# Kernel tuning notes

Hardware: AMD Instinct MI355X
Metric: run time of the kernel (lower is better)

The kernel has to match this reference:

```python
import jax, jax.numpy as jnp
import numpy as np

EPS_NORM = 1e-12  # F.normalize eps
BN_EPS = 1e-5     # BatchNorm2d eps
N_NODES = 18
T_STEPS = 1280
FC_IN = 1469952


def _temporal_conv(x, wa, ba, wb, bb, wc, bc):
    """Gated temporal conv (GLU) from STConv's TemporalConv.
    x: (B, T, N, C) -> (B, T-k+1, N, Cout)."""
    xp = jnp.transpose(x, (0, 3, 2, 1))  # (B, C, N, T)

    def conv(w, b):
        y = jax.lax.conv_general_dilated(
            xp, w, window_strides=(1, 1), padding='VALID',
            dimension_numbers=('NCHW', 'OIHW', 'NCHW'))
        return y + b[None, :, None, None]

    P = conv(wa, ba)
    Q = jax.nn.sigmoid(conv(wb, bb))
    H = jax.nn.relu(P * Q + conv(wc, bc))
    return jnp.transpose(H, (0, 3, 2, 1))  # (B, T', N, Cout)


def setup_inputs() -> dict:
    key = jax.random.key(0)
    ks = jax.random.split(key, 16)
    s = 0.05
    inp = {
        'x': jax.random.normal(ks[0], (N_NODES, 1, T_STEPS), dtype=jnp.float32),
        'edge_index': jax.random.randint(ks[1], (2, 306), 0, N_NODES, dtype=jnp.int64),
        'edge_weight': jax.random.uniform(ks[2], (306,), dtype=jnp.float32),
        'w1a': jax.random.normal(ks[3], (64, 1, 1, 3), dtype=jnp.float32) * s,
        'b1a': jnp.zeros((64,), jnp.float32),
        'w1b': jax.random.normal(ks[4], (64, 1, 1, 3), dtype=jnp.float32) * s,
        'b1b': jnp.zeros((64,), jnp.float32),
        'w1c': jax.random.normal(ks[5], (64, 1, 1, 3), dtype=jnp.float32) * s,
        'b1c': jnp.zeros((64,), jnp.float32),
        'cheb_w': jax.random.normal(ks[6], (64, 64), dtype=jnp.float32) * s,
        'cheb_b': jnp.zeros((64,), jnp.float32),
        'w2a': jax.random.normal(ks[7], (64, 64, 1, 3), dtype=jnp.float32) * s,
        'b2a': jnp.zeros((64,), jnp.float32),
        'w2b': jax.random.normal(ks[8], (64, 64, 1, 3), dtype=jnp.float32) * s,
        'b2b': jnp.zeros((64,), jnp.float32),
        'w2c': jax.random.normal(ks[9], (64, 64, 1, 3), dtype=jnp.float32) * s,
        'b2c': jnp.zeros((64,), jnp.float32),
        'bn_gamma': jnp.ones((N_NODES,), jnp.float32),
        'bn_beta': jnp.zeros((N_NODES,), jnp.float32),
        'fc_w': jax.random.normal(ks[10], (1, FC_IN), dtype=jnp.float32) * 0.001,
        'fc_b': jnp.zeros((1,), jnp.float32),
    }
    return inp


def reference(x, edge_index, edge_weight,
              w1a, b1a, w1b, b1b, w1c, b1c,
              cheb_w, cheb_b,
              w2a, b2a, w2b, b2b, w2c, b2c,
              bn_gamma, bn_beta, fc_w, fc_b):
    # F.normalize(x, dim=1): x shape (N, 1, T)
    norm = jnp.sqrt(jnp.sum(x * x, axis=1, keepdims=True))
    xn = x / jnp.maximum(norm, EPS_NORM)
    # x[None].reshape([1, shape[3], shape[1], shape[2]]): row-major reshape (faithful)
    X = jnp.reshape(xn[None], (1, xn.shape[2], xn.shape[0], xn.shape[1]))  # (1, T, N, 1)

    T0 = _temporal_conv(X, w1a, b1a, w1b, b1b, w1c, b1c)  # (1, T-2, N, 64)
    # ChebConv with K=1: only T_0 = I term -> per-node linear; edge_index/edge_weight unused
    T = jnp.einsum('btnc,cd->btnd', T0, cheb_w) + cheb_b
    T = jax.nn.relu(T)
    T = _temporal_conv(T, w2a, b2a, w2b, b2b, w2c, b2c)  # (1, T-4, N, 64)

    # BatchNorm2d(num_nodes) in training mode: normalize per-node over (B, T, C)
    Tp = jnp.transpose(T, (0, 2, 1, 3))  # (B, N, T, C)
    mean = jnp.mean(Tp, axis=(0, 2, 3), keepdims=True)
    var = jnp.mean((Tp - mean) ** 2, axis=(0, 2, 3), keepdims=True)  # biased var
    Tn = (Tp - mean) / jnp.sqrt(var + BN_EPS)
    Tn = Tn * bn_gamma[None, :, None, None] + bn_beta[None, :, None, None]
    h = jnp.transpose(Tn, (0, 2, 1, 3))  # (B, T-4, N, C)

    h = jax.nn.relu(h).reshape(-1)  # flatten(start_dim=0)
    return fc_w @ h + fc_b  # (1,)
```

## Files before the change

### kernel.cpp

```cpp
#include <hip/hip_runtime.h>
#include <math.h>

#define NN 18
#define T_STEPS 1280
#define T1LEN 1278
#define T2LEN 1276
#define PREPBLK 144
#define TC2 46
#define NCHUNK2 ((T2LEN + TC2 - 1) / TC2)
#define NBLK (NCHUNK2 * NN)

typedef __attribute__((ext_vector_type(8))) short short8;
typedef __attribute__((ext_vector_type(4))) float f32x4;

__device__ __forceinline__ unsigned short f2bf(float v) {
    unsigned u = __builtin_bit_cast(unsigned, v);
    u = u + 0x7fff + ((u >> 16) & 1);
    return (unsigned short)(u >> 16);
}
__device__ __forceinline__ float bf2f(unsigned short h) {
    unsigned u = ((unsigned)h) << 16;
    return __builtin_bit_cast(float, u);
}
__device__ __forceinline__ int swz(int row, int c) {
    return row * 64 + (((c >> 3) ^ (row & 7)) << 3) + (c & 7);
}
__device__ __forceinline__ float ratomic_ld(const float* p) {
    return __hip_atomic_load(p, __ATOMIC_RELAXED, __HIP_MEMORY_SCOPE_AGENT);
}
__device__ __forceinline__ void ratomic_st(float* p, float v) {
    __hip_atomic_store(p, v, __ATOMIC_RELAXED, __HIP_MEMORY_SCOPE_AGENT);
}

__global__ void k_wprep(const float* __restrict__ wa, const float* __restrict__ wb,
                        const float* __restrict__ wc,
                        unsigned short* __restrict__ WBhi, unsigned short* __restrict__ WBlo,
                        int* __restrict__ cnts) {
    int i = blockIdx.x * 256 + threadIdx.x;
    if (blockIdx.x == 0 && threadIdx.x < 38) cnts[threadIdx.x * 32] = 0;
    if (i >= 6 * 192 * 32) return;
    int klocal = i & 31;
    int col = (i >> 5) % 192;
    int kb = i / (192 * 32);
    int conv = col >> 6, co = col & 63;
    int k = kb >> 1, ci = (kb & 1) * 32 + klocal;
    const float* w = (conv == 0) ? wa : (conv == 1 ? wb : wc);
    float v = w[co * 192 + ci * 3 + k];
    unsigned short hi = f2bf(v);
    WBhi[i] = hi;
    WBlo[i] = f2bf(v - bf2f(hi));
}

__global__ __launch_bounds__(256, 2) void k_mega(const float* __restrict__ x,
        const float* __restrict__ w1a, const float* __restrict__ b1a,
        const float* __restrict__ w1b, const float* __restrict__ b1b,
        const float* __restrict__ w1c, const float* __restrict__ b1c,
        const float* __restrict__ cw, const float* __restrict__ cb,
        const unsigned short* __restrict__ WBhi, const unsigned short* __restrict__ WBlo,
        const float* __restrict__ b2a, const float* __restrict__ b2b,
        const float* __restrict__ b2c,
        const float* __restrict__ gamma, const float* __restrict__ beta,
        const float* __restrict__ fcw, const float* __restrict__ fcb,
        float* parts, float* dpart, float* ndot, int* cnts,
        float* __restrict__ out) {
    __shared__ float xs[52];
    __shared__ uint4 t1H[384], t1L[384];
    __shared__ uint4 t2H[400], t2L[400];
    __shared__ float red1[256], red2[256];
    __shared__ float pl[2 * NCHUNK2];
    __shared__ int flagNode, flagAll;
    int b = blockIdx.x;
    int node = b / NCHUNK2, chunk = b % NCHUNK2;
    int t0 = chunk * TC2;
    int tid = threadIdx.x;
    int l = tid & 63, w = tid >> 6;
    int co = w * 16 + (l & 15);
    int* cntA = cnts + node * 32;
    int* cntC = cnts + (19 + node) * 32;
    int* cntD = cnts + 37 * 32;

    float fwreg[12];
    #pragma unroll
    for (int mt = 0; mt < 3; ++mt) {
        #pragma unroll
        for (int r = 0; r < 4; ++r) {
            int tl2 = mt * 16 + (l >> 4) * 4 + r;
            int t = t0 + tl2;
            fwreg[mt * 4 + r] = (tl2 < TC2 && t < T2LEN)
                ? fcw[(t * NN + node) * 64 + co] : 0.f;
        }
    }

    if (tid < 50) {
        int xt = t0 + tid;
        float v = (xt < T_STEPS) ? x[xt * NN + node] : 0.f;
        xs[tid] = v / fmaxf(fabsf(v), 1e-12f);
    }
    __syncthreads();

    {
        unsigned short* tH = (unsigned short*)t1H;
        unsigned short* tL = (unsigned short*)t1L;
        int c = l;
        float wa0 = w1a[c*3], wa1 = w1a[c*3+1], wa2 = w1a[c*3+2];
        float wb0 = w1b[c*3], wb1 = w1b[c*3+1], wb2 = w1b[c*3+2];
        float wc0 = w1c[c*3], wc1 = w1c[c*3+1], wc2 = w1c[c*3+2];
        float ba = b1a[c], bb = b1b[c], bc = b1c[c];
        #pragma unroll
        for (int j = 0; j < 12; ++j) {
            int r = w * 12 + j;
            float x0 = xs[r], x1 = xs[r + 1], x2 = xs[r + 2];
            float pa = fmaf(wa2, x2, fmaf(wa1, x1, fmaf(wa0, x0, ba)));
            float pb = fmaf(wb2, x2, fmaf(wb1, x1, fmaf(wb0, x0, bb)));
            float pc_ = fmaf(wc2, x2, fmaf(wc1, x1, fmaf(wc0, x0, bc)));
            float q = 1.0f / (1.0f + expf(-pb));
            float v = fmaxf(pa * q + pc_, 0.f);
            if (t0 + r >= T1LEN) v = 0.f;
            unsigned short hi = f2bf(v);
            int sw = swz(r, c);
            tH[sw] = hi;
            tL[sw] = f2bf(v - bf2f(hi));
        }
    }
    int d = w * 16 + (l & 15);
    short8 cbh[2], cbl[2];
    #pragma unroll
    for (int kb = 0; kb < 2; ++kb) {
        #pragma unroll
        for (int j = 0; j < 8; ++j) {
            float v = cw[(kb * 32 + (l >> 4) * 8 + j) * 64 + d];
            unsigned short hi = f2bf(v);
            cbh[kb][j] = (short)hi;
            cbl[kb][j] = (short)f2bf(v - bf2f(hi));
        }
    }
    __syncthreads();
    {
        f32x4 acc1[3];
        #pragma unroll
        for (int mt = 0; mt < 3; ++mt) acc1[mt] = (f32x4){0.f,0.f,0.f,0.f};
        #pragma unroll
        for (int kb = 0; kb < 2; ++kb) {
            #pragma unroll
            for (int mt = 0; mt < 3; ++mt) {
                int row = mt * 16 + (l & 15);
                int cbi = kb * 4 + (l >> 4);
                int si = row * 8 + (cbi ^ (row & 7));
                short8 ah = __builtin_bit_cast(short8, t1H[si]);
                short8 al = __builtin_bit_cast(short8, t1L[si]);
                acc1[mt] = __builtin_amdgcn_mfma_f32_16x16x32_bf16(ah, cbh[kb], acc1[mt], 0, 0, 0);
                acc1[mt] = __builtin_amdgcn_mfma_f32_16x16x32_bf16(al, cbh[kb], acc1[mt], 0, 0, 0);
                acc1[mt] = __builtin_amdgcn_mfma_f32_16x16x32_bf16(ah, cbl[kb], acc1[mt], 0, 0, 0);
            }
        }
        float cbias = cb[d];
        unsigned short* tH = (unsigned short*)t2H;
        unsigned short* tL = (unsigned short*)t2L;
        #pragma unroll
        for (int mt = 0; mt < 3; ++mt) {
            #pragma unroll
            for (int r = 0; r < 4; ++r) {
                int row = mt * 16 + (l >> 4) * 4 + r;
                float v = fmaxf(acc1[mt][r] + cbias, 0.f);
                if (t0 + row >= T1LEN) v = 0.f;
                unsigned short hi = f2bf(v);
                int sw = swz(row, d);
                tH[sw] = hi;
                tL[sw] = f2bf(v - bf2f(hi));
            }
        }
        if (tid < 128) {
            int row = 48 + (tid >> 6), c = tid & 63;
            int sw = swz(row, c);
            tH[sw] = 0; tL[sw] = 0;
        }
    }
    __syncthreads();
    float hval[12];
    float s_sum = 0.f, s_sq = 0.f;
    {
        const uint4* wbh = (const uint4*)WBhi;
        const uint4* wbl = (const uint4*)WBlo;
        f32x4 acc[3][3];
        #pragma unroll
        for (int mt = 0; mt < 3; ++mt)
            #pragma unroll
            for (int ct = 0; ct < 3; ++ct)
                acc[mt][ct] = (f32x4){0.f, 0.f, 0.f, 0.f};
        for (int kb = 0; kb < 6; ++kb) {
            short8 bh[3], bl[3];
            #pragma unroll
            for (int ct = 0; ct < 3; ++ct) {
                int col = (w + 4 * ct) * 16 + (l & 15);
                int gi = (kb * 192 + col) * 4 + (l >> 4);
                bh[ct] = __builtin_bit_cast(short8, wbh[gi]);
                bl[ct] = __builtin_bit_cast(short8, wbl[gi]);
            }
            #pragma unroll
            for (int mt = 0; mt < 3; ++mt) {
                int row = mt * 16 + (l & 15) + (kb >> 1);
                int cb2 = (kb & 1) * 4 + (l >> 4);
                int si = row * 8 + (cb2 ^ (row & 7));
                short8 ah = __builtin_bit_cast(short8, t2H[si]);
                short8 al = __builtin_bit_cast(short8, t2L[si]);
                acc[mt][0] = __builtin_amdgcn_mfma_f32_16x16x32_bf16(ah, bh[0], acc[mt][0], 0, 0, 0);
                acc[mt][1] = __builtin_amdgcn_mfma_f32_16x16x32_bf16(ah, bh[1], acc[mt][1], 0, 0, 0);
                acc[mt][2] = __builtin_amdgcn_mfma_f32_16x16x32_bf16(ah, bh[2], acc[mt][2], 0, 0, 0);
                acc[mt][0] = __builtin_amdgcn_mfma_f32_16x16x32_bf16(al, bh[0], acc[mt][0], 0, 0, 0);
                acc[mt][1] = __builtin_amdgcn_mfma_f32_16x16x32_bf16(al, bh[1], acc[mt][1], 0, 0, 0);
                acc[mt][2] = __builtin_amdgcn_mfma_f32_16x16x32_bf16(al, bh[2], acc[mt][2], 0, 0, 0);
                acc[mt][0] = __builtin_amdgcn_mfma_f32_16x16x32_bf16(ah, bl[0], acc[mt][0], 0, 0, 0);
                acc[mt][1] = __builtin_amdgcn_mfma_f32_16x16x32_bf16(ah, bl[1], acc[mt][1], 0, 0, 0);
                acc[mt][2] = __builtin_amdgcn_mfma_f32_16x16x32_bf16(ah, bl[2], acc[mt][2], 0, 0, 0);
            }
        }
        float ba = b2a[co], bb = b2b[co], bc = b2c[co];
        #pragma unroll
        for (int mt = 0; mt < 3; ++mt) {
            #pragma unroll
            for (int r = 0; r < 4; ++r) {
                int tl2 = mt * 16 + (l >> 4) * 4 + r;
                int t = t0 + tl2;
                float hv = 0.f;
                if (tl2 < TC2 && t < T2LEN) {
                    float P = acc[mt][0][r] + ba, Q = acc[mt][1][r] + bb, Cc = acc[mt][2][r] + bc;
                    float qs = 1.f / (1.f + expf(-Q));
                    hv = fmaxf(fmaf(P, qs, Cc), 0.f);
                    s_sum += hv;
                    s_sq = fmaf(hv, hv, s_sq);
                }
                hval[mt * 4 + r] = hv;
            }
        }
    }
    red1[tid] = s_sum; red2[tid] = s_sq;
    __syncthreads();
    for (int off = 128; off > 0; off >>= 1) {
        if (tid < off) { red1[tid] += red1[tid + off]; red2[tid] += red2[tid + off]; }
        __syncthreads();
    }
    if (tid == 0) {
        ratomic_st(&parts[b * 2],     red1[0]);
        ratomic_st(&parts[b * 2 + 1], red2[0]);
        asm volatile("s_waitcnt vmcnt(0)" ::: "memory");
        __hip_atomic_fetch_add(cntA, 1, __ATOMIC_RELAXED, __HIP_MEMORY_SCOPE_AGENT);
        while (__hip_atomic_load(cntA, __ATOMIC_RELAXED, __HIP_MEMORY_SCOPE_AGENT) < NCHUNK2)
            __builtin_amdgcn_s_sleep(4);
    }
    __syncthreads();
    if (tid < 2 * NCHUNK2) pl[tid] = ratomic_ld(&parts[node * 2 * NCHUNK2 + tid]);
    __syncthreads();
    float s = 0.f, q = 0.f;
    #pragma unroll
    for (int i = 0; i < NCHUNK2; ++i) { s += pl[2 * i]; q += pl[2 * i + 1]; }
    float cntf = (float)(T2LEN * 64);
    float mean = s / cntf;
    float var = q / cntf - mean * mean;
    float istd = rsqrtf(var + 1e-5f);
    float g = gamma[node], bt = beta[node];
    float acc = 0.f;
    #pragma unroll
    for (int mt = 0; mt < 3; ++mt) {
        #pragma unroll
        for (int r = 0; r < 4; ++r) {
            int tl2 = mt * 16 + (l >> 4) * 4 + r;
            int t = t0 + tl2;
            if (tl2 < TC2 && t < T2LEN) {
                float v = fmaxf((hval[mt * 4 + r] - mean) * istd * g + bt, 0.f);
                acc = fmaf(v, fwreg[mt * 4 + r], acc);
            }
        }
    }
    red1[tid] = acc;
    __syncthreads();
    for (int off = 128; off > 0; off >>= 1) {
        if (tid < off) red1[tid] += red1[tid + off];
        __syncthreads();
    }
    if (tid == 0) {
        ratomic_st(&dpart[b], red1[0]);
        asm volatile("s_waitcnt vmcnt(0)" ::: "memory");
        int o = __hip_atomic_fetch_add(cntC, 1, __ATOMIC_RELAXED, __HIP_MEMORY_SCOPE_AGENT);
        flagNode = (o == NCHUNK2 - 1);
    }
    __syncthreads();
    if (!flagNode) return;
    {
        float v = (tid < NCHUNK2) ? ratomic_ld(&dpart[node * NCHUNK2 + tid]) : 0.f;
        red1[tid] = v;
        __syncthreads();
        for (int off = 128; off > 0; off >>= 1) {
            if (tid < off) red1[tid] += red1[tid + off];
            __syncthreads();
        }
        if (tid == 0) {
            ratomic_st(&ndot[node], red1[0]);
            asm volatile("s_waitcnt vmcnt(0)" ::: "memory");
            int o2 = __hip_atomic_fetch_add(cntD, 1, __ATOMIC_RELAXED, __HIP_MEMORY_SCOPE_AGENT);
            flagAll = (o2 == NN - 1);
        }
        __syncthreads();
    }
    if (!flagAll) return;
    {
        float v = (tid < NN) ? ratomic_ld(&ndot[tid]) : 0.f;
        red1[tid] = v;
        __syncthreads();
        for (int off = 128; off > 0; off >>= 1) {
            if (tid < off) red1[tid] += red1[tid + off];
            __syncthreads();
        }
        if (tid == 0) out[0] = red1[0] + fcb[0];
    }
}

extern "C" void kernel_launch(void* const* d_in, const int* in_sizes, int n_in,
                              void* d_out, int out_size, void* d_ws, size_t ws_size,
                              hipStream_t stream) {
    const float* x     = (const float*)d_in[0];
    const float* w1a   = (const float*)d_in[3];
    const float* b1a   = (const float*)d_in[4];
    const float* w1b   = (const float*)d_in[5];
    const float* b1b   = (const float*)d_in[6];
    const float* w1c   = (const float*)d_in[7];
    const float* b1c   = (const float*)d_in[8];
    const float* chw   = (const float*)d_in[9];
    const float* chb   = (const float*)d_in[10];
    const float* w2a   = (const float*)d_in[11];
    const float* b2a   = (const float*)d_in[12];
    const float* w2b   = (const float*)d_in[13];
    const float* b2b   = (const float*)d_in[14];
    const float* w2c   = (const float*)d_in[15];
    const float* b2c   = (const float*)d_in[16];
    const float* gamma = (const float*)d_in[17];
    const float* beta  = (const float*)d_in[18];
    const float* fcw   = (const float*)d_in[19];
    const float* fcb   = (const float*)d_in[20];
    float* out = (float*)d_out;

    char* base = (char*)d_ws;
    unsigned short* WBhi  = (unsigned short*)(base);
    unsigned short* WBlo  = (unsigned short*)(base + 73728);
    float*          parts = (float*)(base + 147456);
    float*          dpart = (float*)(base + 151552);
    float*          ndot  = (float*)(base + 153600);
    int*            cnts  = (int*)(base + 153728);

    k_wprep<<<PREPBLK, 256, 0, stream>>>(w2a, w2b, w2c, WBhi, WBlo, cnts);
    k_mega<<<NBLK, 256, 0, stream>>>(
        x, w1a, b1a, w1b, b1b, w1c, b1c, chw, chb,
        WBhi, WBlo, b2a, b2b, b2c, gamma, beta, fcw, fcb,
        parts, dpart, ndot, cnts, out);
}
```

Before: 28.13 us.

## Fold weight-prep kernel into megakernel with counter-based readiness flag

```diff
diff --git a/kernel.cpp b/kernel.cpp
--- a/kernel.cpp
+++ b/kernel.cpp
@@ -5,10 +5,15 @@
 #define T_STEPS 1280
 #define T1LEN 1278
 #define T2LEN 1276
-#define PREPBLK 144
 #define TC2 46
 #define NCHUNK2 ((T2LEN + TC2 - 1) / TC2)
 #define NBLK (NCHUNK2 * NN)
+#define CIDX_ANODE(n) (n)
+#define CIDX_CNODE(n) (18 + (n))
+#define CIDX_D        36
+#define CIDX_WGRP(g)  (37 + (g))
+#define CIDX_WFIN     46
+#define NCNT 47
 
 typedef __attribute__((ext_vector_type(8))) short short8;
 typedef __attribute__((ext_vector_type(4))) float f32x4;
@@ -31,24 +36,14 @@
 __device__ __forceinline__ void ratomic_st(float* p, float v) {
     __hip_atomic_store(p, v, __ATOMIC_RELAXED, __HIP_MEMORY_SCOPE_AGENT);
 }
-
-__global__ void k_wprep(const float* __restrict__ wa, const float* __restrict__ wb,
-                        const float* __restrict__ wc,
-                        unsigned short* __restrict__ WBhi, unsigned short* __restrict__ WBlo,
-                        int* __restrict__ cnts) {
-    int i = blockIdx.x * 256 + threadIdx.x;
-    if (blockIdx.x == 0 && threadIdx.x < 38) cnts[threadIdx.x * 32] = 0;
-    if (i >= 6 * 192 * 32) return;
-    int klocal = i & 31;
-    int col = (i >> 5) % 192;
-    int kb = i / (192 * 32);
-    int conv = col >> 6, co = col & 63;
-    int k = kb >> 1, ci = (kb & 1) * 32 + klocal;
-    const float* w = (conv == 0) ? wa : (conv == 1 ? wb : wc);
-    float v = w[co * 192 + ci * 3 + k];
-    unsigned short hi = f2bf(v);
-    WBhi[i] = hi;
-    WBlo[i] = f2bf(v - bf2f(hi));
+__device__ __forceinline__ void ratomic_stu(unsigned* p, unsigned v) {
+    __hip_atomic_store(p, v, __ATOMIC_RELAXED, __HIP_MEMORY_SCOPE_AGENT);
+}
+__device__ __forceinline__ int radd(int* p) {
+    return __hip_atomic_fetch_add(p, 1, __ATOMIC_RELAXED, __HIP_MEMORY_SCOPE_AGENT);
+}
+__device__ __forceinline__ int rld(const int* p) {
+    return __hip_atomic_load(p, __ATOMIC_RELAXED, __HIP_MEMORY_SCOPE_AGENT);
 }
 
 __global__ __launch_bounds__(256, 2) void k_mega(const float* __restrict__ x,
@@ -56,7 +51,9 @@
         const float* __restrict__ w1b, const float* __restrict__ b1b,
         const float* __restrict__ w1c, const float* __restrict__ b1c,
         const float* __restrict__ cw, const float* __restrict__ cb,
-        const unsigned short* __restrict__ WBhi, const unsigned short* __restrict__ WBlo,
+        const float* __restrict__ w2a, const float* __restrict__ w2b,
+        const float* __restrict__ w2c,
+        unsigned short* __restrict__ WBhi, unsigned short* __restrict__ WBlo,
         const float* __restrict__ b2a, const float* __restrict__ b2b,
         const float* __restrict__ b2c,
         const float* __restrict__ gamma, const float* __restrict__ beta,
@@ -75,10 +72,40 @@
     int tid = threadIdx.x;
     int l = tid & 63, w = tid >> 6;
     int co = w * 16 + (l & 15);
-    int* cntA = cnts + node * 32;
-    int* cntC = cnts + (19 + node) * 32;
-    int* cntD = cnts + 37 * 32;
-
+
+    if (b < 72) {
+        int j = b * 256 + tid;
+        int kh  = j & 15;
+        int col = (j >> 4) % 192;
+        int kb  = j / (192 * 16);
+        int conv = col >> 6, cow = col & 63, k = kb >> 1;
+        const float* wsrc = (conv == 0) ? w2a : (conv == 1 ? w2b : w2c);
+        unsigned hi01 = 0, lo01 = 0;
+        #pragma unroll
+        for (int s2 = 0; s2 < 2; ++s2) {
+            int klocal = 2 * kh + s2;
+            int ci = (kb & 1) * 32 + klocal;
+            float v = wsrc[cow * 192 + ci * 3 + k];
+            unsigned short h = f2bf(v);
+            unsigned short lo = f2bf(v - bf2f(h));
+            hi01 |= ((unsigned)h)  << (16 * s2);
+            lo01 |= ((unsigned)lo) << (16 * s2);
+        }
+        ratomic_stu(&((unsigned*)WBhi)[j], hi01);
+        ratomic_stu(&((unsigned*)WBlo)[j], lo01);
+        asm volatile("s_waitcnt vmcnt(0)" ::: "memory");
+        __syncthreads();
+        if (tid == 0) {
+            int o = radd(&cnts[CIDX_WGRP(b >> 3) * 32]);
+            if (o == 7) radd(&cnts[CIDX_WFIN * 32]);
+        }
+    }
+
+    if (tid < 50) {
+        int xt = t0 + tid;
+        float v = (xt < T_STEPS) ? x[xt * NN + node] : 0.f;
+        xs[tid] = v / fmaxf(fabsf(v), 1e-12f);
+    }
     float fwreg[12];
     #pragma unroll
     for (int mt = 0; mt < 3; ++mt) {
@@ -89,12 +116,6 @@
             fwreg[mt * 4 + r] = (tl2 < TC2 && t < T2LEN)
                 ? fcw[(t * NN + node) * 64 + co] : 0.f;
         }
-    }
-
-    if (tid < 50) {
-        int xt = t0 + tid;
-        float v = (xt < T_STEPS) ? x[xt * NN + node] : 0.f;
-        xs[tid] = v / fmaxf(fabsf(v), 1e-12f);
     }
     __syncthreads();
 
@@ -174,6 +195,11 @@
             int sw = swz(row, c);
             tH[sw] = 0; tL[sw] = 0;
         }
+    }
+    __syncthreads();
+    if (tid == 0) {
+        while (rld(&cnts[CIDX_WFIN * 32]) < 9)
+            __builtin_amdgcn_s_sleep(2);
     }
     __syncthreads();
     float hval[12];
@@ -243,8 +269,8 @@
         ratomic_st(&parts[b * 2],     red1[0]);
         ratomic_st(&parts[b * 2 + 1], red2[0]);
         asm volatile("s_waitcnt vmcnt(0)" ::: "memory");
-        __hip_atomic_fetch_add(cntA, 1, __ATOMIC_RELAXED, __HIP_MEMORY_SCOPE_AGENT);
-        while (__hip_atomic_load(cntA, __ATOMIC_RELAXED, __HIP_MEMORY_SCOPE_AGENT) < NCHUNK2)
+        radd(&cnts[CIDX_ANODE(node) * 32]);
+        while (rld(&cnts[CIDX_ANODE(node) * 32]) < NCHUNK2)
             __builtin_amdgcn_s_sleep(4);
     }
     __syncthreads();
@@ -280,7 +306,7 @@
     if (tid == 0) {
         ratomic_st(&dpart[b], red1[0]);
         asm volatile("s_waitcnt vmcnt(0)" ::: "memory");
-        int o = __hip_atomic_fetch_add(cntC, 1, __ATOMIC_RELAXED, __HIP_MEMORY_SCOPE_AGENT);
+        int o = radd(&cnts[CIDX_CNODE(node) * 32]);
         flagNode = (o == NCHUNK2 - 1);
     }
     __syncthreads();
@@ -296,7 +322,7 @@
         if (tid == 0) {
             ratomic_st(&ndot[node], red1[0]);
             asm volatile("s_waitcnt vmcnt(0)" ::: "memory");
-            int o2 = __hip_atomic_fetch_add(cntD, 1, __ATOMIC_RELAXED, __HIP_MEMORY_SCOPE_AGENT);
+            int o2 = radd(&cnts[CIDX_D * 32]);
             flagAll = (o2 == NN - 1);
         }
         __syncthreads();
@@ -346,9 +372,9 @@
     float*          ndot  = (float*)(base + 153600);
     int*            cnts  = (int*)(base + 153728);
 
-    k_wprep<<<PREPBLK, 256, 0, stream>>>(w2a, w2b, w2c, WBhi, WBlo, cnts);
+    hipMemsetAsync(cnts, 0, NCNT * 128, stream);
     k_mega<<<NBLK, 256, 0, stream>>>(
         x, w1a, b1a, w1b, b1b, w1c, b1c, chw, chb,
-        WBhi, WBlo, b2a, b2b, b2c, gamma, beta, fcw, fcb,
+        w2a, w2b, w2c, WBhi, WBlo, b2a, b2b, b2c, gamma, beta, fcw, fcb,
         parts, dpart, ndot, cnts, out);
 }
```

Result: slower. 29.42 us (+4.6%).
